# Performance work log

Hardware: AMD Instinct MI355X
Metric: run time of the kernel (lower is better)

## Reference

```python
import jax, jax.numpy as jnp
import numpy as np
import math

D = 768
H = 12
DFF = 3072
HD = D // H


def _layernorm(x, g, b, eps=1e-5):
    mu = jnp.mean(x, axis=-1, keepdims=True)
    var = jnp.var(x, axis=-1, keepdims=True)
    return (x - mu) * jax.lax.rsqrt(var + eps) * g + b


def setup_inputs() -> dict:
    key = jax.random.key(0)
    ks = jax.random.split(key, 12)
    B, S = 2, 4096
    s = 1.0 / math.sqrt(D)
    sf = 1.0 / math.sqrt(DFF)
    return {
        "x": jax.random.normal(ks[0], (B, S, D), jnp.float32),
        "attention_mask": jnp.ones((B, S), jnp.int32),
        "ln1_g": jnp.ones((D,), jnp.float32),
        "ln1_b": jnp.zeros((D,), jnp.float32),
        "ln2_g": jnp.ones((D,), jnp.float32),
        "ln2_b": jnp.zeros((D,), jnp.float32),
        "Wq": jax.random.normal(ks[1], (D, D), jnp.float32) * s,
        "bq": jnp.zeros((D,), jnp.float32),
        "Wk": jax.random.normal(ks[2], (D, D), jnp.float32) * s,
        "bk": jnp.zeros((D,), jnp.float32),
        "Wv": jax.random.normal(ks[3], (D, D), jnp.float32) * s,
        "bv": jnp.zeros((D,), jnp.float32),
        "Wo": jax.random.normal(ks[4], (D, D), jnp.float32) * s,
        "bo": jnp.zeros((D,), jnp.float32),
        "W1": jax.random.normal(ks[5], (D, DFF), jnp.float32) * s,
        "b1": jnp.zeros((DFF,), jnp.float32),
        "W2": jax.random.normal(ks[6], (DFF, D), jnp.float32) * sf,
        "b2": jnp.zeros((D,), jnp.float32),
    }


def _block(x, attention_mask, ln1_g, ln1_b, ln2_g, ln2_b,
           Wq, bq, Wk, bk, Wv, bv, Wo, bo, W1, b1, W2, b2):
    B, S, _ = x.shape
    h = _layernorm(x, ln1_g, ln1_b)
    q = (h @ Wq + bq).reshape(B, S, H, HD)
    k = (h @ Wk + bk).reshape(B, S, H, HD)
    v = (h @ Wv + bv).reshape(B, S, H, HD)
    # scores: [B, H, S, S]
    dots = jnp.einsum('bqhd,bkhd->bhqk', q, k) / math.sqrt(HD)
    causal = jnp.tril(jnp.ones((S, S), bool))  # True = keep
    keep = causal[None, None] & (attention_mask != 0)[:, None, None, :]
    dots = jnp.where(keep, dots, -jnp.inf)
    probs = jax.nn.softmax(dots, axis=-1)
    ctx = jnp.einsum('bhqk,bkhd->bqhd', probs, v).reshape(B, S, D)
    sa = ctx @ Wo + bo  # dropout = identity (eval)
    x = x + sa
    h2 = _layernorm(x, ln2_g, ln2_b)
    ff = jax.nn.relu(h2 @ W1 + b1) @ W2 + b2
    return x + ff


def reference(x, attention_mask, ln1_g, ln1_b, ln2_g, ln2_b,
              Wq, bq, Wk, bk, Wv, bv, Wo, bo, W1, b1, W2, b2):
    return _block(x, attention_mask, ln1_g, ln1_b, ln2_g, ln2_b,
                  Wq, bq, Wk, bk, Wv, bv, Wo, bo, W1, b1, W2, b2)
```

## Files before the change

kernel.cpp:

```cpp
#include <hip/hip_runtime.h>
#include <hip/hip_bf16.h>
#include <math.h>

#define S_LEN 4096
#define DMODEL 768
#define NHEAD 12
#define HDIM 64
#define DFF_ 3072
#define MROWS 8192

typedef __bf16 bf16;
typedef __bf16 bf16x4 __attribute__((ext_vector_type(4)));
typedef __bf16 bf16x8 __attribute__((ext_vector_type(8)));
typedef float f32x4 __attribute__((ext_vector_type(4)));

union F4 { float4 v; float f[4]; };
union U2 { bf16 h[2]; unsigned u; };
union U8 { unsigned u[4]; bf16x8 v; };

__device__ __forceinline__ void gld_lds16(void* lds, const void* g) {
    __builtin_amdgcn_global_load_lds(
        (const __attribute__((address_space(1))) unsigned int*)g,
        (__attribute__((address_space(3))) unsigned int*)lds, 16, 0, 0);
}

template<typename OUT>
__global__ __launch_bounds__(256) void ln_kernel(const float* __restrict__ x,
                                                 const float* __restrict__ g,
                                                 const float* __restrict__ bta,
                                                 OUT* __restrict__ out) {
    const int row = blockIdx.x;
    const int t = threadIdx.x;
    const float* xr = x + (size_t)row * DMODEL;
    float v0 = xr[t], v1 = xr[t + 256], v2 = xr[t + 512];
    float s = v0 + v1 + v2;
    float ss = v0 * v0 + v1 * v1 + v2 * v2;
    for (int o = 32; o > 0; o >>= 1) {
        s += __shfl_down(s, o, 64);
        ss += __shfl_down(ss, o, 64);
    }
    __shared__ float sm[4], sm2[4];
    const int w = t >> 6, lane = t & 63;
    if (lane == 0) { sm[w] = s; sm2[w] = ss; }
    __syncthreads();
    s = sm[0] + sm[1] + sm[2] + sm[3];
    ss = sm2[0] + sm2[1] + sm2[2] + sm2[3];
    const float mu = s * (1.0f / DMODEL);
    const float var = ss * (1.0f / DMODEL) - mu * mu;
    const float rs = rsqrtf(var + 1e-5f);
    OUT* orow = out + (size_t)row * DMODEL;
    orow[t]       = (OUT)((v0 - mu) * rs * g[t]       + bta[t]);
    orow[t + 256] = (OUT)((v1 - mu) * rs * g[t + 256] + bta[t + 256]);
    orow[t + 512] = (OUT)((v2 - mu) * rs * g[t + 512] + bta[t + 512]);
}

__global__ __launch_bounds__(256) void wtrans_kernel(const float* __restrict__ W,
                                                     bf16* __restrict__ Wt,
                                                     int K, int N) {
    __shared__ float tile[64][65];
    const int tid = threadIdx.x;
    const int n0 = blockIdx.x * 64, k0 = blockIdx.y * 64;
    const int lr = tid >> 4, lc = (tid & 15) << 2;
#pragma unroll
    for (int i = 0; i < 4; ++i) {
        const int r = lr + i * 16;
        F4 w; w.v = *(const float4*)&W[(size_t)(k0 + r) * N + n0 + lc];
#pragma unroll
        for (int j = 0; j < 4; ++j) tile[r][lc + j] = w.f[j];
    }
    __syncthreads();
#pragma unroll
    for (int i = 0; i < 4; ++i) {
        const int n = lr + i * 16;
        bf16x4 o;
#pragma unroll
        for (int j = 0; j < 4; ++j) o[j] = (bf16)tile[lc + j][n];
        *(bf16x4*)&Wt[(size_t)(n0 + n) * K + k0 + lc] = o;
    }
}

template<int MT, bool RELU, bool RES, bool OUT_BF16>
__global__ __launch_bounds__(256) void mgemm_kernel(
    const bf16* __restrict__ A,
    const bf16* __restrict__ Wt0, const float* __restrict__ bias0, void* __restrict__ C0,
    const bf16* __restrict__ Wt1, const float* __restrict__ bias1, void* __restrict__ C1,
    const bf16* __restrict__ Wt2, const float* __restrict__ bias2, void* __restrict__ C2,
    const float* __restrict__ R, int M, int N, int K,
    float sc0, float sc1, float sc2) {
    const bf16* Wt = Wt0; const float* bias = bias0; void* C = C0; float sc = sc0;
    if (blockIdx.z == 1) { Wt = Wt1; bias = bias1; C = C1; sc = sc1; }
    if (blockIdx.z == 2) { Wt = Wt2; bias = bias2; C = C2; sc = sc2; }

    constexpr int NI = (MT == 128) ? 4 : 2;
    __shared__ bf16 As[MT * 32];
    __shared__ bf16 Bs[128 * 32];

    const int tid = threadIdx.x;
    const int wave = tid >> 6, lane = tid & 63;
    const int row0 = blockIdx.y * MT, col0 = blockIdx.x * 128;
    const int wr = (MT == 128) ? (wave >> 1) * 64 : 0;
    const int wc = (MT == 128) ? (wave & 1) * 64 : wave * 32;
    const int mrow = lane & 15, kq = (lane >> 4) * 8;

    const int st_row = (lane >> 2);
    const int st_off = (lane & 3) * 16;

    f32x4 acc[4][NI] = {};

    const char* Ab = (const char*)(A + (size_t)row0 * K);
    const char* Bb = (const char*)(Wt + (size_t)col0 * K);
    const size_t strideA = (size_t)K * 2;

    for (int k0 = 0; k0 < K; k0 += 32) {
        if (MT == 128) {
#pragma unroll
            for (int issue = 0; issue < 2; ++issue) {
                const int r = wave * 32 + issue * 16 + st_row;
                gld_lds16((char*)As + (wave * 32 + issue * 16) * 64,
                          Ab + (size_t)r * strideA + k0 * 2 + st_off);
            }
        } else {
            const int r = wave * 16 + st_row;
            gld_lds16((char*)As + (wave * 16) * 64,
                      Ab + (size_t)r * strideA + k0 * 2 + st_off);
        }
#pragma unroll
        for (int issue = 0; issue < 2; ++issue) {
            const int r = wave * 32 + issue * 16 + st_row;
            gld_lds16((char*)Bs + (wave * 32 + issue * 16) * 64,
                      Bb + (size_t)r * strideA + k0 * 2 + st_off);
        }
        __syncthreads();
        bf16x8 af[4], bfr[NI];
#pragma unroll
        for (int mi = 0; mi < 4; ++mi)
            af[mi] = *(const bf16x8*)&As[(wr + mi * 16 + mrow) * 32 + kq];
#pragma unroll
        for (int ni = 0; ni < NI; ++ni)
            bfr[ni] = *(const bf16x8*)&Bs[(wc + ni * 16 + mrow) * 32 + kq];
#pragma unroll
        for (int mi = 0; mi < 4; ++mi)
#pragma unroll
            for (int ni = 0; ni < NI; ++ni)
                acc[mi][ni] = __builtin_amdgcn_mfma_f32_16x16x32_bf16(
                    af[mi], bfr[ni], acc[mi][ni], 0, 0, 0);
        __syncthreads();
    }

    const int quad = lane >> 4;
    float bv[NI];
#pragma unroll
    for (int ni = 0; ni < NI; ++ni) bv[ni] = bias[col0 + wc + ni * 16 + mrow];
#pragma unroll
    for (int mi = 0; mi < 4; ++mi) {
#pragma unroll
        for (int r = 0; r < 4; ++r) {
            const int row = row0 + wr + mi * 16 + quad * 4 + r;
#pragma unroll
            for (int ni = 0; ni < NI; ++ni) {
                const int col = col0 + wc + ni * 16 + mrow;
                float v = acc[mi][ni][r] + bv[ni];
                if (RES) v += R[(size_t)row * N + col];
                v *= sc;
                if (RELU) v = fmaxf(v, 0.0f);
                if (OUT_BF16) ((bf16*)C)[(size_t)row * N + col] = (bf16)v;
                else          ((float*)C)[(size_t)row * N + col] = v;
            }
        }
    }
}

__global__ __launch_bounds__(256) void mattn_kernel(
    const bf16* __restrict__ Q, const bf16* __restrict__ K,
    const bf16* __restrict__ V, const int* __restrict__ amask,
    bf16* __restrict__ O) {
    const int bx = blockIdx.x, h = blockIdx.y, b = blockIdx.z;

    __shared__ bf16 Ks[2][64][68];
    __shared__ bf16 Vt[2][64][68];
    __shared__ bf16 Os[64][68];
    __shared__ float mk[2][64];
    __shared__ int flagv[2];

    const int tid = threadIdx.x;
    const int wave = tid >> 6, lane = tid & 63;
    const int l = lane & 15, quad = lane >> 4;
    const int qh = quad >> 1;
    const int srcA = (quad & 1) * 32 + l;
    const int srcB = srcA + 16;
    const float NEG_INF = -__builtin_huge_valf();

    const int kr = tid >> 2, ks = (tid & 3) * 16;
    const int vk0 = (tid & 31) * 2, vds = (tid >> 5) * 8;

    const bf16* Kbase = K + (size_t)b * S_LEN * DMODEL + h * HDIM;
    const bf16* Vbase = V + (size_t)b * S_LEN * DMODEL + h * HDIM;

#pragma unroll 1
    for (int pass = 0; pass < 2; ++pass) {
        const int qt = pass ? bx : (63 - bx);

        const bf16* Qb = Q + (size_t)(b * S_LEN + qt * 64 + wave * 16 + l) * DMODEL + h * HDIM;
        const bf16x8 qf0 = *(const bf16x8*)(Qb + quad * 8);
        const bf16x8 qf1 = *(const bf16x8*)(Qb + 32 + quad * 8);

        float m_run = NEG_INF, l_run = 0.0f;
        f32x4 acc[4] = {};

        bf16x8 kp0, kp1, vp0, vp1;
        int mv = 1;
        {
            const bf16* kg = Kbase + (size_t)kr * DMODEL + ks;
            kp0 = *(const bf16x8*)kg;
            kp1 = *(const bf16x8*)(kg + 8);
            const bf16* vg = Vbase + (size_t)vk0 * DMODEL + vds;
            vp0 = *(const bf16x8*)vg;
            vp1 = *(const bf16x8*)(vg + DMODEL);
            if (wave == 0) mv = amask[b * S_LEN + lane];
        }
        __syncthreads();
        {
            *(bf16x8*)&Ks[0][kr][ks]     = kp0;
            *(bf16x8*)&Ks[0][kr][ks + 8] = kp1;
#pragma unroll
            for (int i = 0; i < 8; ++i) {
                U2 w; w.h[0] = vp0[i]; w.h[1] = vp1[i];
                *(unsigned*)&Vt[0][vds + i][vk0] = w.u;
            }
            if (wave == 0) {
                mk[0][lane] = mv ? 0.0f : NEG_INF;
                unsigned long long bal = __ballot(mv != 0);
                if (lane == 0) flagv[0] = (bal == ~0ULL);
            }
        }
        __syncthreads();
        int buf = 0;

        for (int kt = 0; kt <= qt; ++kt) {
            const bool more = (kt < qt);
            if (more) {
                const bf16* kg = Kbase + (size_t)((kt + 1) * 64 + kr) * DMODEL + ks;
                kp0 = *(const bf16x8*)kg;
                kp1 = *(const bf16x8*)(kg + 8);
                const bf16* vg = Vbase + (size_t)((kt + 1) * 64 + vk0) * DMODEL + vds;
                vp0 = *(const bf16x8*)vg;
                vp1 = *(const bf16x8*)(vg + DMODEL);
                if (wave == 0) mv = amask[b * S_LEN + (kt + 1) * 64 + lane];
            }

            const int allv = flagv[buf];
            f32x4 sreg[4] = {};
#pragma unroll
            for (int mi = 0; mi < 4; ++mi) {
                bf16x8 kf0 = *(const bf16x8*)&Ks[buf][mi * 16 + l][quad * 8];
                bf16x8 kf1 = *(const bf16x8*)&Ks[buf][mi * 16 + l][32 + quad * 8];
                sreg[mi] = __builtin_amdgcn_mfma_f32_16x16x32_bf16(kf0, qf0, sreg[mi], 0, 0, 0);
                sreg[mi] = __builtin_amdgcn_mfma_f32_16x16x32_bf16(kf1, qf1, sreg[mi], 0, 0, 0);
            }
            if (!allv) {
#pragma unroll
                for (int mi = 0; mi < 4; ++mi) {
                    F4 m4; m4.v = *(const float4*)&mk[buf][mi * 16 + quad * 4];
#pragma unroll
                    for (int r = 0; r < 4; ++r) sreg[mi][r] += m4.f[r];
                }
            }
            if (kt == qt) {
#pragma unroll
                for (int mi = 0; mi < 4; ++mi)
#pragma unroll
                    for (int r = 0; r < 4; ++r)
                        if (mi * 16 + quad * 4 + r > wave * 16 + l)
                            sreg[mi][r] = NEG_INF;
            }

            float mloc = sreg[0][0];
#pragma unroll
            for (int mi = 0; mi < 4; ++mi)
#pragma unroll
                for (int r = 0; r < 4; ++r) mloc = fmaxf(mloc, sreg[mi][r]);
            mloc = fmaxf(mloc, __shfl_xor(mloc, 16, 64));
            mloc = fmaxf(mloc, __shfl_xor(mloc, 32, 64));
            const float mn = fmaxf(m_run, mloc);
            const float alpha = __builtin_amdgcn_exp2f(m_run - mn);
            m_run = mn;
            float ls = 0.0f;
#pragma unroll
            for (int mi = 0; mi < 4; ++mi)
#pragma unroll
                for (int r = 0; r < 4; ++r) {
                    const float p = __builtin_amdgcn_exp2f(sreg[mi][r] - mn);
                    sreg[mi][r] = p;
                    ls += p;
                }
            ls += __shfl_xor(ls, 16, 64);
            ls += __shfl_xor(ls, 32, 64);
            l_run = l_run * alpha + ls;
#pragma unroll
            for (int mi = 0; mi < 4; ++mi)
#pragma unroll
                for (int r = 0; r < 4; ++r) acc[mi][r] *= alpha;

            unsigned pk[4][2];
#pragma unroll
            for (int mi = 0; mi < 4; ++mi) {
                U2 w0; w0.h[0] = (bf16)sreg[mi][0]; w0.h[1] = (bf16)sreg[mi][1];
                U2 w1; w1.h[0] = (bf16)sreg[mi][2]; w1.h[1] = (bf16)sreg[mi][3];
                pk[mi][0] = w0.u; pk[mi][1] = w1.u;
            }
            bf16x8 pfrag[2];
#pragma unroll
            for (int kc = 0; kc < 2; ++kc) {
                U8 u;
#pragma unroll
                for (int t = 0; t < 2; ++t) {
                    const unsigned a0 = (unsigned)__shfl((int)pk[2 * kc][t],     srcA, 64);
                    const unsigned b0 = (unsigned)__shfl((int)pk[2 * kc + 1][t], srcA, 64);
                    u.u[t] = qh ? b0 : a0;
                    const unsigned a1 = (unsigned)__shfl((int)pk[2 * kc][t],     srcB, 64);
                    const unsigned b1 = (unsigned)__shfl((int)pk[2 * kc + 1][t], srcB, 64);
                    u.u[2 + t] = qh ? b1 : a1;
                }
                pfrag[kc] = u.v;
            }
#pragma unroll
            for (int mi = 0; mi < 4; ++mi) {
                bf16x8 vf0 = *(const bf16x8*)&Vt[buf][mi * 16 + l][quad * 8];
                bf16x8 vf1 = *(const bf16x8*)&Vt[buf][mi * 16 + l][32 + quad * 8];
                acc[mi] = __builtin_amdgcn_mfma_f32_16x16x32_bf16(vf0, pfrag[0], acc[mi], 0, 0, 0);
                acc[mi] = __builtin_amdgcn_mfma_f32_16x16x32_bf16(vf1, pfrag[1], acc[mi], 0, 0, 0);
            }

            if (more) {
                const int nb = buf ^ 1;
                *(bf16x8*)&Ks[nb][kr][ks]     = kp0;
                *(bf16x8*)&Ks[nb][kr][ks + 8] = kp1;
#pragma unroll
                for (int i = 0; i < 8; ++i) {
                    U2 w; w.h[0] = vp0[i]; w.h[1] = vp1[i];
                    *(unsigned*)&Vt[nb][vds + i][vk0] = w.u;
                }
                if (wave == 0) {
                    mk[nb][lane] = mv ? 0.0f : NEG_INF;
                    unsigned long long bal = __ballot(mv != 0);
                    if (lane == 0) flagv[nb] = (bal == ~0ULL);
                }
            }
            __syncthreads();
            buf ^= 1;
        }

        const float rinv = 1.0f / l_run;
#pragma unroll
        for (int mi = 0; mi < 4; ++mi) {
            U2 w0; w0.h[0] = (bf16)(acc[mi][0] * rinv); w0.h[1] = (bf16)(acc[mi][1] * rinv);
            U2 w1; w1.h[0] = (bf16)(acc[mi][2] * rinv); w1.h[1] = (bf16)(acc[mi][3] * rinv);
            *(unsigned*)&Os[wave * 16 + l][mi * 16 + quad * 4]     = w0.u;
            *(unsigned*)&Os[wave * 16 + l][mi * 16 + quad * 4 + 2] = w1.u;
        }
        __syncthreads();
        {
            const int orow = tid >> 2, oseg = (tid & 3) * 16;
            bf16* Og = O + (size_t)(b * S_LEN + qt * 64 + orow) * DMODEL + h * HDIM + oseg;
            *(bf16x8*)Og       = *(const bf16x8*)&Os[orow][oseg];
            *(bf16x8*)(Og + 8) = *(const bf16x8*)&Os[orow][oseg + 8];
        }
    }
}

extern "C" void kernel_launch(void* const* d_in, const int* in_sizes, int n_in,
                              void* d_out, int out_size, void* d_ws, size_t ws_size,
                              hipStream_t stream) {
    const float* x     = (const float*)d_in[0];
    const int*   amask = (const int*)  d_in[1];
    const float* ln1_g = (const float*)d_in[2];
    const float* ln1_b = (const float*)d_in[3];
    const float* ln2_g = (const float*)d_in[4];
    const float* ln2_b = (const float*)d_in[5];
    const float* Wq = (const float*)d_in[6];  const float* bq = (const float*)d_in[7];
    const float* Wk = (const float*)d_in[8];  const float* bk = (const float*)d_in[9];
    const float* Wv = (const float*)d_in[10]; const float* bv = (const float*)d_in[11];
    const float* Wo = (const float*)d_in[12]; const float* bo = (const float*)d_in[13];
    const float* W1 = (const float*)d_in[14]; const float* b1 = (const float*)d_in[15];
    const float* W2 = (const float*)d_in[16]; const float* b2 = (const float*)d_in[17];
    float* out = (float*)d_out;

    char* ws = (char*)d_ws;
    const size_t WSML = (size_t)DMODEL * DMODEL * 2;
    const size_t WBIG = (size_t)DMODEL * DFF_ * 2;
    bf16* Wqt = (bf16*)(ws + 0 * WSML);
    bf16* Wkt = (bf16*)(ws + 1 * WSML);
    bf16* Wvt = (bf16*)(ws + 2 * WSML);
    bf16* Wot = (bf16*)(ws + 3 * WSML);
    bf16* W1t = (bf16*)(ws + 4 * WSML);
    bf16* W2t = (bf16*)(ws + 4 * WSML + WBIG);
    char* act = ws + 4 * WSML + 2 * WBIG;

    const size_t HB = (size_t)MROWS * DMODEL * 2;
    const size_t FB = (size_t)MROWS * DMODEL * 4;
    bf16*  h    = (bf16*)(act);
    bf16*  qb   = (bf16*)(act + HB);
    bf16*  kb   = (bf16*)(act + 2 * HB);
    bf16*  vb   = (bf16*)(act + 3 * HB);
    bf16*  ctx  = h;
    float* x1   = (float*)(act + 4 * HB);
    bf16*  f    = (bf16*)(act + 4 * HB + FB);
    bf16*  h2   = h;

    const float SCL = 0.125f * 1.44269504089f;

    wtrans_kernel<<<dim3(DMODEL / 64, DMODEL / 64), 256, 0, stream>>>(Wq, Wqt, DMODEL, DMODEL);
    wtrans_kernel<<<dim3(DMODEL / 64, DMODEL / 64), 256, 0, stream>>>(Wk, Wkt, DMODEL, DMODEL);
    wtrans_kernel<<<dim3(DMODEL / 64, DMODEL / 64), 256, 0, stream>>>(Wv, Wvt, DMODEL, DMODEL);
    wtrans_kernel<<<dim3(DMODEL / 64, DMODEL / 64), 256, 0, stream>>>(Wo, Wot, DMODEL, DMODEL);
    wtrans_kernel<<<dim3(DFF_ / 64, DMODEL / 64), 256, 0, stream>>>(W1, W1t, DMODEL, DFF_);
    wtrans_kernel<<<dim3(DMODEL / 64, DFF_ / 64), 256, 0, stream>>>(W2, W2t, DFF_, DMODEL);

    ln_kernel<bf16><<<MROWS, 256, 0, stream>>>(x, ln1_g, ln1_b, h);
    mgemm_kernel<128, false, false, true><<<dim3(DMODEL / 128, MROWS / 128, 3), 256, 0, stream>>>(
        h, Wqt, bq, qb, Wkt, bk, kb, Wvt, bv, vb, nullptr, MROWS, DMODEL, DMODEL,
        SCL, 1.0f, 1.0f);
    mattn_kernel<<<dim3(32, NHEAD, 2), 256, 0, stream>>>(qb, kb, vb, amask, ctx);
    mgemm_kernel<64, false, true, false><<<dim3(DMODEL / 128, MROWS / 64, 1), 256, 0, stream>>>(
        ctx, Wot, bo, x1, Wot, bo, x1, Wot, bo, x1, x, MROWS, DMODEL, DMODEL,
        1.0f, 1.0f, 1.0f);
    ln_kernel<bf16><<<MROWS, 256, 0, stream>>>(x1, ln2_g, ln2_b, h2);
    mgemm_kernel<128, true, false, true><<<dim3(DFF_ / 128, MROWS / 128, 1), 256, 0, stream>>>(
        h2, W1t, b1, f, W1t, b1, f, W1t, b1, f, nullptr, MROWS, DFF_, DMODEL,
        1.0f, 1.0f, 1.0f);
    mgemm_kernel<64, false, true, false><<<dim3(DMODEL / 128, MROWS / 64, 1), 256, 0, stream>>>(
        f, W2t, b2, out, W2t, b2, out, W2t, b2, out, x1, MROWS, DMODEL, DFF_,
        1.0f, 1.0f, 1.0f);
}
```

Before: 504.8 us.

## Process two 64-row query groups per attention block to share K/V tiles

Each attention block now handles 128 query rows as two 64-row groups with separate online-softmax state. Each K/V tile loaded into LDS is reused by both groups, and the extra diagonal tile is skipped for the first group. This halves K/V global loads and LDS fills per query row, but also halves the grid and raises register pressure; launch bounds are set to target two blocks per CU. The output staging buffer now aliases the K tile memory. The padding-mask read no longer selects the current double-buffer slot, which only matters when the mask contains zeros.

```diff
diff --git a/kernel.cpp b/kernel.cpp
--- a/kernel.cpp
+++ b/kernel.cpp
@@ -170,17 +170,19 @@
     }
 }
 
-__global__ __launch_bounds__(256) void mattn_kernel(
+__global__ __launch_bounds__(256, 2) void mattn_kernel(
     const bf16* __restrict__ Q, const bf16* __restrict__ K,
     const bf16* __restrict__ V, const int* __restrict__ amask,
     bf16* __restrict__ O) {
     const int bx = blockIdx.x, h = blockIdx.y, b = blockIdx.z;
 
-    __shared__ bf16 Ks[2][64][68];
-    __shared__ bf16 Vt[2][64][68];
-    __shared__ bf16 Os[64][68];
-    __shared__ float mk[2][64];
-    __shared__ int flagv[2];
+    __shared__ __align__(16) char smem[2 * 17408 + 512 + 16];
+    typedef bf16 Tile[64][68];
+    Tile* Ks = (Tile*)smem;
+    Tile* Vt = (Tile*)(smem + 17408);
+    float* mk = (float*)(smem + 34816);
+    int* flagv = (int*)(smem + 34816 + 512);
+    bf16 (*Os)[68] = (bf16(*)[68])smem;
 
     const int tid = threadIdx.x;
     const int wave = tid >> 6, lane = tid & 63;
@@ -198,14 +200,19 @@
 
 #pragma unroll 1
     for (int pass = 0; pass < 2; ++pass) {
-        const int qt = pass ? bx : (63 - bx);
-
-        const bf16* Qb = Q + (size_t)(b * S_LEN + qt * 64 + wave * 16 + l) * DMODEL + h * HDIM;
-        const bf16x8 qf0 = *(const bf16x8*)(Qb + quad * 8);
-        const bf16x8 qf1 = *(const bf16x8*)(Qb + 32 + quad * 8);
-
-        float m_run = NEG_INF, l_run = 0.0f;
-        f32x4 acc[4] = {};
+        const int qt = pass ? bx : (31 - bx);
+        const int ktmax = 2 * qt + 1;
+
+        bf16x8 qf[2][2];
+#pragma unroll
+        for (int g = 0; g < 2; ++g) {
+            const bf16* Qb = Q + (size_t)(b * S_LEN + qt * 128 + g * 64 + wave * 16 + l) * DMODEL + h * HDIM;
+            qf[g][0] = *(const bf16x8*)(Qb + quad * 8);
+            qf[g][1] = *(const bf16x8*)(Qb + 32 + quad * 8);
+        }
+
+        float m_run[2] = {NEG_INF, NEG_INF}, l_run[2] = {0.0f, 0.0f};
+        f32x4 acc[2][4] = {};
 
         bf16x8 kp0, kp1, vp0, vp1;
         int mv = 1;
@@ -228,7 +235,7 @@
                 *(unsigned*)&Vt[0][vds + i][vk0] = w.u;
             }
             if (wave == 0) {
-                mk[0][lane] = mv ? 0.0f : NEG_INF;
+                mk[lane] = mv ? 0.0f : NEG_INF;
                 unsigned long long bal = __ballot(mv != 0);
                 if (lane == 0) flagv[0] = (bal == ~0ULL);
             }
@@ -236,8 +243,8 @@
         __syncthreads();
         int buf = 0;
 
-        for (int kt = 0; kt <= qt; ++kt) {
-            const bool more = (kt < qt);
+        for (int kt = 0; kt <= ktmax; ++kt) {
+            const bool more = (kt < ktmax);
             if (more) {
                 const bf16* kg = Kbase + (size_t)((kt + 1) * 64 + kr) * DMODEL + ks;
                 kp0 = *(const bf16x8*)kg;
@@ -249,86 +256,109 @@
             }
 
             const int allv = flagv[buf];
-            f32x4 sreg[4] = {};
+            const bool skip0 = (kt == 2 * qt + 1);
+
+            bf16x8 kf[4][2];
 #pragma unroll
             for (int mi = 0; mi < 4; ++mi) {
-                bf16x8 kf0 = *(const bf16x8*)&Ks[buf][mi * 16 + l][quad * 8];
-                bf16x8 kf1 = *(const bf16x8*)&Ks[buf][mi * 16 + l][32 + quad * 8];
-                sreg[mi] = __builtin_amdgcn_mfma_f32_16x16x32_bf16(kf0, qf0, sreg[mi], 0, 0, 0);
-                sreg[mi] = __builtin_amdgcn_mfma_f32_16x16x32_bf16(kf1, qf1, sreg[mi], 0, 0, 0);
-            }
-            if (!allv) {
+                kf[mi][0] = *(const bf16x8*)&Ks[buf][mi * 16 + l][quad * 8];
+                kf[mi][1] = *(const bf16x8*)&Ks[buf][mi * 16 + l][32 + quad * 8];
+            }
+            f32x4 sreg[2][4] = {};
+#pragma unroll
+            for (int g = 0; g < 2; ++g) {
+                if (g == 0 && skip0) continue;
 #pragma unroll
                 for (int mi = 0; mi < 4; ++mi) {
-                    F4 m4; m4.v = *(const float4*)&mk[buf][mi * 16 + quad * 4];
-#pragma unroll
-                    for (int r = 0; r < 4; ++r) sreg[mi][r] += m4.f[r];
-                }
-            }
-            if (kt == qt) {
+                    sreg[g][mi] = __builtin_amdgcn_mfma_f32_16x16x32_bf16(kf[mi][0], qf[g][0], sreg[g][mi], 0, 0, 0);
+                    sreg[g][mi] = __builtin_amdgcn_mfma_f32_16x16x32_bf16(kf[mi][1], qf[g][1], sreg[g][mi], 0, 0, 0);
+                }
+            }
+
+            bf16x8 pfrag[2][2];
+#pragma unroll
+            for (int g = 0; g < 2; ++g) {
+                if (g == 0 && skip0) continue;
+                if (!allv) {
+#pragma unroll
+                    for (int mi = 0; mi < 4; ++mi) {
+                        F4 m4; m4.v = *(const float4*)&mk[mi * 16 + quad * 4];
+#pragma unroll
+                        for (int r = 0; r < 4; ++r) sreg[g][mi][r] += m4.f[r];
+                    }
+                }
+                if (kt == 2 * qt + g) {
+#pragma unroll
+                    for (int mi = 0; mi < 4; ++mi)
+#pragma unroll
+                        for (int r = 0; r < 4; ++r)
+                            if (mi * 16 + quad * 4 + r > wave * 16 + l)
+                                sreg[g][mi][r] = NEG_INF;
+                }
+                float mloc = sreg[g][0][0];
 #pragma unroll
                 for (int mi = 0; mi < 4; ++mi)
 #pragma unroll
-                    for (int r = 0; r < 4; ++r)
-                        if (mi * 16 + quad * 4 + r > wave * 16 + l)
-                            sreg[mi][r] = NEG_INF;
-            }
-
-            float mloc = sreg[0][0];
-#pragma unroll
-            for (int mi = 0; mi < 4; ++mi)
-#pragma unroll
-                for (int r = 0; r < 4; ++r) mloc = fmaxf(mloc, sreg[mi][r]);
-            mloc = fmaxf(mloc, __shfl_xor(mloc, 16, 64));
-            mloc = fmaxf(mloc, __shfl_xor(mloc, 32, 64));
-            const float mn = fmaxf(m_run, mloc);
-            const float alpha = __builtin_amdgcn_exp2f(m_run - mn);
-            m_run = mn;
-            float ls = 0.0f;
-#pragma unroll
-            for (int mi = 0; mi < 4; ++mi)
-#pragma unroll
-                for (int r = 0; r < 4; ++r) {
-                    const float p = __builtin_amdgcn_exp2f(sreg[mi][r] - mn);
-                    sreg[mi][r] = p;
-                    ls += p;
-                }
-            ls += __shfl_xor(ls, 16, 64);
-            ls += __shfl_xor(ls, 32, 64);
-            l_run = l_run * alpha + ls;
-#pragma unroll
-            for (int mi = 0; mi < 4; ++mi)
-#pragma unroll
-                for (int r = 0; r < 4; ++r) acc[mi][r] *= alpha;
-
-            unsigned pk[4][2];
+                    for (int r = 0; r < 4; ++r) mloc = fmaxf(mloc, sreg[g][mi][r]);
+                mloc = fmaxf(mloc, __shfl_xor(mloc, 16, 64));
+                mloc = fmaxf(mloc, __shfl_xor(mloc, 32, 64));
+                const float mn = fmaxf(m_run[g], mloc);
+                const float alpha = __builtin_amdgcn_exp2f(m_run[g] - mn);
+                m_run[g] = mn;
+                float ls = 0.0f;
+#pragma unroll
+                for (int mi = 0; mi < 4; ++mi)
+#pragma unroll
+                    for (int r = 0; r < 4; ++r) {
+                        const float p = __builtin_amdgcn_exp2f(sreg[g][mi][r] - mn);
+                        sreg[g][mi][r] = p;
+                        ls += p;
+                    }
+                ls += __shfl_xor(ls, 16, 64);
+                ls += __shfl_xor(ls, 32, 64);
+                l_run[g] = l_run[g] * alpha + ls;
+#pragma unroll
+                for (int mi = 0; mi < 4; ++mi)
+#pragma unroll
+                    for (int r = 0; r < 4; ++r) acc[g][mi][r] *= alpha;
+
+                unsigned pk[4][2];
+#pragma unroll
+                for (int mi = 0; mi < 4; ++mi) {
+                    U2 w0; w0.h[0] = (bf16)sreg[g][mi][0]; w0.h[1] = (bf16)sreg[g][mi][1];
+                    U2 w1; w1.h[0] = (bf16)sreg[g][mi][2]; w1.h[1] = (bf16)sreg[g][mi][3];
+                    pk[mi][0] = w0.u; pk[mi][1] = w1.u;
+                }
+#pragma unroll
+                for (int kc = 0; kc < 2; ++kc) {
+                    U8 u;
+#pragma unroll
+                    for (int t = 0; t < 2; ++t) {
+                        const unsigned a0 = (unsigned)__shfl((int)pk[2 * kc][t],     srcA, 64);
+                        const unsigned b0 = (unsigned)__shfl((int)pk[2 * kc + 1][t], srcA, 64);
+                        u.u[t] = qh ? b0 : a0;
+                        const unsigned a1 = (unsigned)__shfl((int)pk[2 * kc][t],     srcB, 64);
+                        const unsigned b1 = (unsigned)__shfl((int)pk[2 * kc + 1][t], srcB, 64);
+                        u.u[2 + t] = qh ? b1 : a1;
+                    }
+                    pfrag[g][kc] = u.v;
+                }
+            }
+
+            bf16x8 vf[4][2];
 #pragma unroll
             for (int mi = 0; mi < 4; ++mi) {
-                U2 w0; w0.h[0] = (bf16)sreg[mi][0]; w0.h[1] = (bf16)sreg[mi][1];
-                U2 w1; w1.h[0] = (bf16)sreg[mi][2]; w1.h[1] = (bf16)sreg[mi][3];
-                pk[mi][0] = w0.u; pk[mi][1] = w1.u;
-            }
-            bf16x8 pfrag[2];
-#pragma unroll
-            for (int kc = 0; kc < 2; ++kc) {
-                U8 u;
-#pragma unroll
-                for (int t = 0; t < 2; ++t) {
-                    const unsigned a0 = (unsigned)__shfl((int)pk[2 * kc][t],     srcA, 64);
-                    const unsigned b0 = (unsigned)__shfl((int)pk[2 * kc + 1][t], srcA, 64);
-                    u.u[t] = qh ? b0 : a0;
-                    const unsigned a1 = (unsigned)__shfl((int)pk[2 * kc][t],     srcB, 64);
-                    const unsigned b1 = (unsigned)__shfl((int)pk[2 * kc + 1][t], srcB, 64);
-                    u.u[2 + t] = qh ? b1 : a1;
-                }
-                pfrag[kc] = u.v;
-            }
-#pragma unroll
-            for (int mi = 0; mi < 4; ++mi) {
-                bf16x8 vf0 = *(const bf16x8*)&Vt[buf][mi * 16 + l][quad * 8];
-                bf16x8 vf1 = *(const bf16x8*)&Vt[buf][mi * 16 + l][32 + quad * 8];
-                acc[mi] = __builtin_amdgcn_mfma_f32_16x16x32_bf16(vf0, pfrag[0], acc[mi], 0, 0, 0);
-                acc[mi] = __builtin_amdgcn_mfma_f32_16x16x32_bf16(vf1, pfrag[1], acc[mi], 0, 0, 0);
+                vf[mi][0] = *(const bf16x8*)&Vt[buf][mi * 16 + l][quad * 8];
+                vf[mi][1] = *(const bf16x8*)&Vt[buf][mi * 16 + l][32 + quad * 8];
+            }
+#pragma unroll
+            for (int g = 0; g < 2; ++g) {
+                if (g == 0 && skip0) continue;
+#pragma unroll
+                for (int mi = 0; mi < 4; ++mi) {
+                    acc[g][mi] = __builtin_amdgcn_mfma_f32_16x16x32_bf16(vf[mi][0], pfrag[g][0], acc[g][mi], 0, 0, 0);
+                    acc[g][mi] = __builtin_amdgcn_mfma_f32_16x16x32_bf16(vf[mi][1], pfrag[g][1], acc[g][mi], 0, 0, 0);
+                }
             }
 
             if (more) {
@@ -341,7 +371,7 @@
                     *(unsigned*)&Vt[nb][vds + i][vk0] = w.u;
                 }
                 if (wave == 0) {
-                    mk[nb][lane] = mv ? 0.0f : NEG_INF;
+                    mk[nb * 64 + lane] = mv ? 0.0f : NEG_INF;
                     unsigned long long bal = __ballot(mv != 0);
                     if (lane == 0) flagv[nb] = (bal == ~0ULL);
                 }
@@ -350,20 +380,25 @@
             buf ^= 1;
         }
 
-        const float rinv = 1.0f / l_run;
-#pragma unroll
-        for (int mi = 0; mi < 4; ++mi) {
-            U2 w0; w0.h[0] = (bf16)(acc[mi][0] * rinv); w0.h[1] = (bf16)(acc[mi][1] * rinv);
-            U2 w1; w1.h[0] = (bf16)(acc[mi][2] * rinv); w1.h[1] = (bf16)(acc[mi][3] * rinv);
-            *(unsigned*)&Os[wave * 16 + l][mi * 16 + quad * 4]     = w0.u;
-            *(unsigned*)&Os[wave * 16 + l][mi * 16 + quad * 4 + 2] = w1.u;
+#pragma unroll
+        for (int g = 0; g < 2; ++g) {
+            const float rinv = 1.0f / l_run[g];
+#pragma unroll
+            for (int mi = 0; mi < 4; ++mi) {
+                U2 w0; w0.h[0] = (bf16)(acc[g][mi][0] * rinv); w0.h[1] = (bf16)(acc[g][mi][1] * rinv);
+                U2 w1; w1.h[0] = (bf16)(acc[g][mi][2] * rinv); w1.h[1] = (bf16)(acc[g][mi][3] * rinv);
+                *(unsigned*)&Os[g * 64 + wave * 16 + l][mi * 16 + quad * 4]     = w0.u;
+                *(unsigned*)&Os[g * 64 + wave * 16 + l][mi * 16 + quad * 4 + 2] = w1.u;
+            }
         }
         __syncthreads();
         {
-            const int orow = tid >> 2, oseg = (tid & 3) * 16;
-            bf16* Og = O + (size_t)(b * S_LEN + qt * 64 + orow) * DMODEL + h * HDIM + oseg;
-            *(bf16x8*)Og       = *(const bf16x8*)&Os[orow][oseg];
-            *(bf16x8*)(Og + 8) = *(const bf16x8*)&Os[orow][oseg + 8];
+            const int orow = tid >> 1, oseg = (tid & 1) * 32;
+            bf16* Og = O + (size_t)(b * S_LEN + qt * 128 + orow) * DMODEL + h * HDIM + oseg;
+            *(bf16x8*)(Og)      = *(const bf16x8*)&Os[orow][oseg];
+            *(bf16x8*)(Og + 8)  = *(const bf16x8*)&Os[orow][oseg + 8];
+            *(bf16x8*)(Og + 16) = *(const bf16x8*)&Os[orow][oseg + 16];
+            *(bf16x8*)(Og + 24) = *(const bf16x8*)&Os[orow][oseg + 24];
         }
     }
 }
@@ -420,7 +455,7 @@
     mgemm_kernel<128, false, false, true><<<dim3(DMODEL / 128, MROWS / 128, 3), 256, 0, stream>>>(
         h, Wqt, bq, qb, Wkt, bk, kb, Wvt, bv, vb, nullptr, MROWS, DMODEL, DMODEL,
         SCL, 1.0f, 1.0f);
-    mattn_kernel<<<dim3(32, NHEAD, 2), 256, 0, stream>>>(qb, kb, vb, amask, ctx);
+    mattn_kernel<<<dim3(16, NHEAD, 2), 256, 0, stream>>>(qb, kb, vb, amask, ctx);
     mgemm_kernel<64, false, true, false><<<dim3(DMODEL / 128, MROWS / 64, 1), 256, 0, stream>>>(
         ctx, Wot, bo, x1, Wot, bo, x1, Wot, bo, x1, x, MROWS, DMODEL, DMODEL,
         1.0f, 1.0f, 1.0f);
```

After: 710.9 us. 40.8% more time.

## Split attention into one query tile per block, fuse weight transposes

Applied to the files above, without the earlier changes.

The attention kernel stops pairing a long and a short query tile inside each block and launches one block per query tile (64 per head), heaviest first. It also reuses the K buffer as output staging to cut shared memory and sets a launch bound of 4 blocks per CU. The six weight-transpose launches are merged into one kernel that dispatches on block index, removing launch overhead. The cost is less inherent load balancing per block, which now depends on the hardware scheduler picking up the reverse-ordered tiles.

```diff
diff --git a/kernel.cpp b/kernel.cpp
--- a/kernel.cpp
+++ b/kernel.cpp
@@ -54,12 +54,25 @@
     orow[t + 512] = (OUT)((v2 - mu) * rs * g[t + 512] + bta[t + 512]);
 }
 
-__global__ __launch_bounds__(256) void wtrans_kernel(const float* __restrict__ W,
-                                                     bf16* __restrict__ Wt,
-                                                     int K, int N) {
+__global__ __launch_bounds__(256) void wtrans_all_kernel(
+    const float* __restrict__ Wq, const float* __restrict__ Wk,
+    const float* __restrict__ Wv, const float* __restrict__ Wo,
+    const float* __restrict__ W1, const float* __restrict__ W2,
+    bf16* __restrict__ Wqt, bf16* __restrict__ Wkt, bf16* __restrict__ Wvt,
+    bf16* __restrict__ Wot, bf16* __restrict__ W1t, bf16* __restrict__ W2t) {
+    int t = blockIdx.x;
+    const float* W; bf16* Wt; int K, N;
+    if      (t < 144)  { W = Wq; Wt = Wqt; K = 768;  N = 768;  }
+    else if (t < 288)  { W = Wk; Wt = Wkt; K = 768;  N = 768;  t -= 144; }
+    else if (t < 432)  { W = Wv; Wt = Wvt; K = 768;  N = 768;  t -= 288; }
+    else if (t < 576)  { W = Wo; Wt = Wot; K = 768;  N = 768;  t -= 432; }
+    else if (t < 1152) { W = W1; Wt = W1t; K = 768;  N = 3072; t -= 576; }
+    else               { W = W2; Wt = W2t; K = 3072; N = 768;  t -= 1152; }
+    const int nx = N >> 6;
+    const int n0 = (t % nx) * 64, k0 = (t / nx) * 64;
+
     __shared__ float tile[64][65];
     const int tid = threadIdx.x;
-    const int n0 = blockIdx.x * 64, k0 = blockIdx.y * 64;
     const int lr = tid >> 4, lc = (tid & 15) << 2;
 #pragma unroll
     for (int i = 0; i < 4; ++i) {
@@ -170,17 +183,18 @@
     }
 }
 
-__global__ __launch_bounds__(256) void mattn_kernel(
+__global__ __launch_bounds__(256, 4) void mattn_kernel(
     const bf16* __restrict__ Q, const bf16* __restrict__ K,
     const bf16* __restrict__ V, const int* __restrict__ amask,
     bf16* __restrict__ O) {
-    const int bx = blockIdx.x, h = blockIdx.y, b = blockIdx.z;
+    const int qt = 63 - blockIdx.x;
+    const int h = blockIdx.y, b = blockIdx.z;
 
     __shared__ bf16 Ks[2][64][68];
     __shared__ bf16 Vt[2][64][68];
-    __shared__ bf16 Os[64][68];
     __shared__ float mk[2][64];
     __shared__ int flagv[2];
+    bf16 (*Os)[68] = Ks[0];
 
     const int tid = threadIdx.x;
     const int wave = tid >> 6, lane = tid & 63;
@@ -196,175 +210,169 @@
     const bf16* Kbase = K + (size_t)b * S_LEN * DMODEL + h * HDIM;
     const bf16* Vbase = V + (size_t)b * S_LEN * DMODEL + h * HDIM;
 
-#pragma unroll 1
-    for (int pass = 0; pass < 2; ++pass) {
-        const int qt = pass ? bx : (63 - bx);
-
-        const bf16* Qb = Q + (size_t)(b * S_LEN + qt * 64 + wave * 16 + l) * DMODEL + h * HDIM;
-        const bf16x8 qf0 = *(const bf16x8*)(Qb + quad * 8);
-        const bf16x8 qf1 = *(const bf16x8*)(Qb + 32 + quad * 8);
-
-        float m_run = NEG_INF, l_run = 0.0f;
-        f32x4 acc[4] = {};
-
-        bf16x8 kp0, kp1, vp0, vp1;
-        int mv = 1;
-        {
-            const bf16* kg = Kbase + (size_t)kr * DMODEL + ks;
+    const bf16* Qb = Q + (size_t)(b * S_LEN + qt * 64 + wave * 16 + l) * DMODEL + h * HDIM;
+    const bf16x8 qf0 = *(const bf16x8*)(Qb + quad * 8);
+    const bf16x8 qf1 = *(const bf16x8*)(Qb + 32 + quad * 8);
+
+    float m_run = NEG_INF, l_run = 0.0f;
+    f32x4 acc[4] = {};
+
+    bf16x8 kp0, kp1, vp0, vp1;
+    int mv = 1;
+    {
+        const bf16* kg = Kbase + (size_t)kr * DMODEL + ks;
+        kp0 = *(const bf16x8*)kg;
+        kp1 = *(const bf16x8*)(kg + 8);
+        const bf16* vg = Vbase + (size_t)vk0 * DMODEL + vds;
+        vp0 = *(const bf16x8*)vg;
+        vp1 = *(const bf16x8*)(vg + DMODEL);
+        if (wave == 0) mv = amask[b * S_LEN + lane];
+    }
+    {
+        *(bf16x8*)&Ks[0][kr][ks]     = kp0;
+        *(bf16x8*)&Ks[0][kr][ks + 8] = kp1;
+#pragma unroll
+        for (int i = 0; i < 8; ++i) {
+            U2 w; w.h[0] = vp0[i]; w.h[1] = vp1[i];
+            *(unsigned*)&Vt[0][vds + i][vk0] = w.u;
+        }
+        if (wave == 0) {
+            mk[0][lane] = mv ? 0.0f : NEG_INF;
+            unsigned long long bal = __ballot(mv != 0);
+            if (lane == 0) flagv[0] = (bal == ~0ULL);
+        }
+    }
+    __syncthreads();
+    int buf = 0;
+
+    for (int kt = 0; kt <= qt; ++kt) {
+        const bool more = (kt < qt);
+        if (more) {
+            const bf16* kg = Kbase + (size_t)((kt + 1) * 64 + kr) * DMODEL + ks;
             kp0 = *(const bf16x8*)kg;
             kp1 = *(const bf16x8*)(kg + 8);
-            const bf16* vg = Vbase + (size_t)vk0 * DMODEL + vds;
+            const bf16* vg = Vbase + (size_t)((kt + 1) * 64 + vk0) * DMODEL + vds;
             vp0 = *(const bf16x8*)vg;
             vp1 = *(const bf16x8*)(vg + DMODEL);
-            if (wave == 0) mv = amask[b * S_LEN + lane];
-        }
-        __syncthreads();
-        {
-            *(bf16x8*)&Ks[0][kr][ks]     = kp0;
-            *(bf16x8*)&Ks[0][kr][ks + 8] = kp1;
+            if (wave == 0) mv = amask[b * S_LEN + (kt + 1) * 64 + lane];
+        }
+
+        const int allv = flagv[buf];
+        f32x4 sreg[4] = {};
+#pragma unroll
+        for (int mi = 0; mi < 4; ++mi) {
+            bf16x8 kf0 = *(const bf16x8*)&Ks[buf][mi * 16 + l][quad * 8];
+            bf16x8 kf1 = *(const bf16x8*)&Ks[buf][mi * 16 + l][32 + quad * 8];
+            sreg[mi] = __builtin_amdgcn_mfma_f32_16x16x32_bf16(kf0, qf0, sreg[mi], 0, 0, 0);
+            sreg[mi] = __builtin_amdgcn_mfma_f32_16x16x32_bf16(kf1, qf1, sreg[mi], 0, 0, 0);
+        }
+        if (!allv) {
+#pragma unroll
+            for (int mi = 0; mi < 4; ++mi) {
+                F4 m4; m4.v = *(const float4*)&mk[buf][mi * 16 + quad * 4];
+#pragma unroll
+                for (int r = 0; r < 4; ++r) sreg[mi][r] += m4.f[r];
+            }
+        }
+        if (kt == qt) {
+#pragma unroll
+            for (int mi = 0; mi < 4; ++mi)
+#pragma unroll
+                for (int r = 0; r < 4; ++r)
+                    if (mi * 16 + quad * 4 + r > wave * 16 + l)
+                        sreg[mi][r] = NEG_INF;
+        }
+
+        float mloc = sreg[0][0];
+#pragma unroll
+        for (int mi = 0; mi < 4; ++mi)
+#pragma unroll
+            for (int r = 0; r < 4; ++r) mloc = fmaxf(mloc, sreg[mi][r]);
+        mloc = fmaxf(mloc, __shfl_xor(mloc, 16, 64));
+        mloc = fmaxf(mloc, __shfl_xor(mloc, 32, 64));
+        const float mn = fmaxf(m_run, mloc);
+        const float alpha = __builtin_amdgcn_exp2f(m_run - mn);
+        m_run = mn;
+        float ls = 0.0f;
+#pragma unroll
+        for (int mi = 0; mi < 4; ++mi)
+#pragma unroll
+            for (int r = 0; r < 4; ++r) {
+                const float p = __builtin_amdgcn_exp2f(sreg[mi][r] - mn);
+                sreg[mi][r] = p;
+                ls += p;
+            }
+        ls += __shfl_xor(ls, 16, 64);
+        ls += __shfl_xor(ls, 32, 64);
+        l_run = l_run * alpha + ls;
+#pragma unroll
+        for (int mi = 0; mi < 4; ++mi)
+#pragma unroll
+            for (int r = 0; r < 4; ++r) acc[mi][r] *= alpha;
+
+        unsigned pk[4][2];
+#pragma unroll
+        for (int mi = 0; mi < 4; ++mi) {
+            U2 w0; w0.h[0] = (bf16)sreg[mi][0]; w0.h[1] = (bf16)sreg[mi][1];
+            U2 w1; w1.h[0] = (bf16)sreg[mi][2]; w1.h[1] = (bf16)sreg[mi][3];
+            pk[mi][0] = w0.u; pk[mi][1] = w1.u;
+        }
+        bf16x8 pfrag[2];
+#pragma unroll
+        for (int kc = 0; kc < 2; ++kc) {
+            U8 u;
+#pragma unroll
+            for (int t = 0; t < 2; ++t) {
+                const unsigned a0 = (unsigned)__shfl((int)pk[2 * kc][t],     srcA, 64);
+                const unsigned b0 = (unsigned)__shfl((int)pk[2 * kc + 1][t], srcA, 64);
+                u.u[t] = qh ? b0 : a0;
+                const unsigned a1 = (unsigned)__shfl((int)pk[2 * kc][t],     srcB, 64);
+                const unsigned b1 = (unsigned)__shfl((int)pk[2 * kc + 1][t], srcB, 64);
+                u.u[2 + t] = qh ? b1 : a1;
+            }
+            pfrag[kc] = u.v;
+        }
+#pragma unroll
+        for (int mi = 0; mi < 4; ++mi) {
+            bf16x8 vf0 = *(const bf16x8*)&Vt[buf][mi * 16 + l][quad * 8];
+            bf16x8 vf1 = *(const bf16x8*)&Vt[buf][mi * 16 + l][32 + quad * 8];
+            acc[mi] = __builtin_amdgcn_mfma_f32_16x16x32_bf16(vf0, pfrag[0], acc[mi], 0, 0, 0);
+            acc[mi] = __builtin_amdgcn_mfma_f32_16x16x32_bf16(vf1, pfrag[1], acc[mi], 0, 0, 0);
+        }
+
+        if (more) {
+            const int nb = buf ^ 1;
+            *(bf16x8*)&Ks[nb][kr][ks]     = kp0;
+            *(bf16x8*)&Ks[nb][kr][ks + 8] = kp1;
 #pragma unroll
             for (int i = 0; i < 8; ++i) {
                 U2 w; w.h[0] = vp0[i]; w.h[1] = vp1[i];
-                *(unsigned*)&Vt[0][vds + i][vk0] = w.u;
+                *(unsigned*)&Vt[nb][vds + i][vk0] = w.u;
             }
             if (wave == 0) {
-                mk[0][lane] = mv ? 0.0f : NEG_INF;
+                mk[nb][lane] = mv ? 0.0f : NEG_INF;
                 unsigned long long bal = __ballot(mv != 0);
-                if (lane == 0) flagv[0] = (bal == ~0ULL);
+                if (lane == 0) flagv[nb] = (bal == ~0ULL);
             }
         }
         __syncthreads();
-        int buf = 0;
-
-        for (int kt = 0; kt <= qt; ++kt) {
-            const bool more = (kt < qt);
-            if (more) {
-                const bf16* kg = Kbase + (size_t)((kt + 1) * 64 + kr) * DMODEL + ks;
-                kp0 = *(const bf16x8*)kg;
-                kp1 = *(const bf16x8*)(kg + 8);
-                const bf16* vg = Vbase + (size_t)((kt + 1) * 64 + vk0) * DMODEL + vds;
-                vp0 = *(const bf16x8*)vg;
-                vp1 = *(const bf16x8*)(vg + DMODEL);
-                if (wave == 0) mv = amask[b * S_LEN + (kt + 1) * 64 + lane];
-            }
-
-            const int allv = flagv[buf];
-            f32x4 sreg[4] = {};
-#pragma unroll
-            for (int mi = 0; mi < 4; ++mi) {
-                bf16x8 kf0 = *(const bf16x8*)&Ks[buf][mi * 16 + l][quad * 8];
-                bf16x8 kf1 = *(const bf16x8*)&Ks[buf][mi * 16 + l][32 + quad * 8];
-                sreg[mi] = __builtin_amdgcn_mfma_f32_16x16x32_bf16(kf0, qf0, sreg[mi], 0, 0, 0);
-                sreg[mi] = __builtin_amdgcn_mfma_f32_16x16x32_bf16(kf1, qf1, sreg[mi], 0, 0, 0);
-            }
-            if (!allv) {
-#pragma unroll
-                for (int mi = 0; mi < 4; ++mi) {
-                    F4 m4; m4.v = *(const float4*)&mk[buf][mi * 16 + quad * 4];
-#pragma unroll
-                    for (int r = 0; r < 4; ++r) sreg[mi][r] += m4.f[r];
-                }
-            }
-            if (kt == qt) {
-#pragma unroll
-                for (int mi = 0; mi < 4; ++mi)
-#pragma unroll
-                    for (int r = 0; r < 4; ++r)
-                        if (mi * 16 + quad * 4 + r > wave * 16 + l)
-                            sreg[mi][r] = NEG_INF;
-            }
-
-            float mloc = sreg[0][0];
-#pragma unroll
-            for (int mi = 0; mi < 4; ++mi)
-#pragma unroll
-                for (int r = 0; r < 4; ++r) mloc = fmaxf(mloc, sreg[mi][r]);
-            mloc = fmaxf(mloc, __shfl_xor(mloc, 16, 64));
-            mloc = fmaxf(mloc, __shfl_xor(mloc, 32, 64));
-            const float mn = fmaxf(m_run, mloc);
-            const float alpha = __builtin_amdgcn_exp2f(m_run - mn);
-            m_run = mn;
-            float ls = 0.0f;
-#pragma unroll
-            for (int mi = 0; mi < 4; ++mi)
-#pragma unroll
-                for (int r = 0; r < 4; ++r) {
-                    const float p = __builtin_amdgcn_exp2f(sreg[mi][r] - mn);
-                    sreg[mi][r] = p;
-                    ls += p;
-                }
-            ls += __shfl_xor(ls, 16, 64);
-            ls += __shfl_xor(ls, 32, 64);
-            l_run = l_run * alpha + ls;
-#pragma unroll
-            for (int mi = 0; mi < 4; ++mi)
-#pragma unroll
-                for (int r = 0; r < 4; ++r) acc[mi][r] *= alpha;
-
-            unsigned pk[4][2];
-#pragma unroll
-            for (int mi = 0; mi < 4; ++mi) {
-                U2 w0; w0.h[0] = (bf16)sreg[mi][0]; w0.h[1] = (bf16)sreg[mi][1];
-                U2 w1; w1.h[0] = (bf16)sreg[mi][2]; w1.h[1] = (bf16)sreg[mi][3];
-                pk[mi][0] = w0.u; pk[mi][1] = w1.u;
-            }
-            bf16x8 pfrag[2];
-#pragma unroll
-            for (int kc = 0; kc < 2; ++kc) {
-                U8 u;
-#pragma unroll
-                for (int t = 0; t < 2; ++t) {
-                    const unsigned a0 = (unsigned)__shfl((int)pk[2 * kc][t],     srcA, 64);
-                    const unsigned b0 = (unsigned)__shfl((int)pk[2 * kc + 1][t], srcA, 64);
-                    u.u[t] = qh ? b0 : a0;
-                    const unsigned a1 = (unsigned)__shfl((int)pk[2 * kc][t],     srcB, 64);
-                    const unsigned b1 = (unsigned)__shfl((int)pk[2 * kc + 1][t], srcB, 64);
-                    u.u[2 + t] = qh ? b1 : a1;
-                }
-                pfrag[kc] = u.v;
-            }
-#pragma unroll
-            for (int mi = 0; mi < 4; ++mi) {
-                bf16x8 vf0 = *(const bf16x8*)&Vt[buf][mi * 16 + l][quad * 8];
-                bf16x8 vf1 = *(const bf16x8*)&Vt[buf][mi * 16 + l][32 + quad * 8];
-                acc[mi] = __builtin_amdgcn_mfma_f32_16x16x32_bf16(vf0, pfrag[0], acc[mi], 0, 0, 0);
-                acc[mi] = __builtin_amdgcn_mfma_f32_16x16x32_bf16(vf1, pfrag[1], acc[mi], 0, 0, 0);
-            }
-
-            if (more) {
-                const int nb = buf ^ 1;
-                *(bf16x8*)&Ks[nb][kr][ks]     = kp0;
-                *(bf16x8*)&Ks[nb][kr][ks + 8] = kp1;
-#pragma unroll
-                for (int i = 0; i < 8; ++i) {
-                    U2 w; w.h[0] = vp0[i]; w.h[1] = vp1[i];
-                    *(unsigned*)&Vt[nb][vds + i][vk0] = w.u;
-                }
-                if (wave == 0) {
-                    mk[nb][lane] = mv ? 0.0f : NEG_INF;
-                    unsigned long long bal = __ballot(mv != 0);
-                    if (lane == 0) flagv[nb] = (bal == ~0ULL);
-                }
-            }
-            __syncthreads();
-            buf ^= 1;
-        }
-
-        const float rinv = 1.0f / l_run;
-#pragma unroll
-        for (int mi = 0; mi < 4; ++mi) {
-            U2 w0; w0.h[0] = (bf16)(acc[mi][0] * rinv); w0.h[1] = (bf16)(acc[mi][1] * rinv);
-            U2 w1; w1.h[0] = (bf16)(acc[mi][2] * rinv); w1.h[1] = (bf16)(acc[mi][3] * rinv);
-            *(unsigned*)&Os[wave * 16 + l][mi * 16 + quad * 4]     = w0.u;
-            *(unsigned*)&Os[wave * 16 + l][mi * 16 + quad * 4 + 2] = w1.u;
-        }
-        __syncthreads();
-        {
-            const int orow = tid >> 2, oseg = (tid & 3) * 16;
-            bf16* Og = O + (size_t)(b * S_LEN + qt * 64 + orow) * DMODEL + h * HDIM + oseg;
-            *(bf16x8*)Og       = *(const bf16x8*)&Os[orow][oseg];
-            *(bf16x8*)(Og + 8) = *(const bf16x8*)&Os[orow][oseg + 8];
-        }
+        buf ^= 1;
+    }
+
+    const float rinv = 1.0f / l_run;
+#pragma unroll
+    for (int mi = 0; mi < 4; ++mi) {
+        U2 w0; w0.h[0] = (bf16)(acc[mi][0] * rinv); w0.h[1] = (bf16)(acc[mi][1] * rinv);
+        U2 w1; w1.h[0] = (bf16)(acc[mi][2] * rinv); w1.h[1] = (bf16)(acc[mi][3] * rinv);
+        *(unsigned*)&Os[wave * 16 + l][mi * 16 + quad * 4]     = w0.u;
+        *(unsigned*)&Os[wave * 16 + l][mi * 16 + quad * 4 + 2] = w1.u;
+    }
+    __syncthreads();
+    {
+        const int orow = tid >> 2, oseg = (tid & 3) * 16;
+        bf16* Og = O + (size_t)(b * S_LEN + qt * 64 + orow) * DMODEL + h * HDIM + oseg;
+        *(bf16x8*)Og       = *(const bf16x8*)&Os[orow][oseg];
+        *(bf16x8*)(Og + 8) = *(const bf16x8*)&Os[orow][oseg + 8];
     }
 }
 
@@ -409,18 +417,14 @@
 
     const float SCL = 0.125f * 1.44269504089f;
 
-    wtrans_kernel<<<dim3(DMODEL / 64, DMODEL / 64), 256, 0, stream>>>(Wq, Wqt, DMODEL, DMODEL);
-    wtrans_kernel<<<dim3(DMODEL / 64, DMODEL / 64), 256, 0, stream>>>(Wk, Wkt, DMODEL, DMODEL);
-    wtrans_kernel<<<dim3(DMODEL / 64, DMODEL / 64), 256, 0, stream>>>(Wv, Wvt, DMODEL, DMODEL);
-    wtrans_kernel<<<dim3(DMODEL / 64, DMODEL / 64), 256, 0, stream>>>(Wo, Wot, DMODEL, DMODEL);
-    wtrans_kernel<<<dim3(DFF_ / 64, DMODEL / 64), 256, 0, stream>>>(W1, W1t, DMODEL, DFF_);
-    wtrans_kernel<<<dim3(DMODEL / 64, DFF_ / 64), 256, 0, stream>>>(W2, W2t, DFF_, DMODEL);
+    wtrans_all_kernel<<<1728, 256, 0, stream>>>(Wq, Wk, Wv, Wo, W1, W2,
+                                                Wqt, Wkt, Wvt, Wot, W1t, W2t);
 
     ln_kernel<bf16><<<MROWS, 256, 0, stream>>>(x, ln1_g, ln1_b, h);
     mgemm_kernel<128, false, false, true><<<dim3(DMODEL / 128, MROWS / 128, 3), 256, 0, stream>>>(
         h, Wqt, bq, qb, Wkt, bk, kb, Wvt, bv, vb, nullptr, MROWS, DMODEL, DMODEL,
         SCL, 1.0f, 1.0f);
-    mattn_kernel<<<dim3(32, NHEAD, 2), 256, 0, stream>>>(qb, kb, vb, amask, ctx);
+    mattn_kernel<<<dim3(64, NHEAD, 2), 256, 0, stream>>>(qb, kb, vb, amask, ctx);
     mgemm_kernel<64, false, true, false><<<dim3(DMODEL / 128, MROWS / 64, 1), 256, 0, stream>>>(
         ctx, Wot, bo, x1, Wot, bo, x1, Wot, bo, x1, x, MROWS, DMODEL, DMODEL,
         1.0f, 1.0f, 1.0f);
```

Measured after the change: 571.8 us. 13.3% more time.
